# Kernel optimization log

Hardware: AMD Instinct MI355X
Metric: run time of the kernel (lower is better)

The kernel has to match this reference:

```python
import jax, jax.numpy as jnp
import numpy as np

N_NODES = 100000
N_EDGES = 1600000
D_IN = 64
D_OUT = 64
BN_EPS = 1e-5


def setup_inputs() -> dict:
    key = jax.random.key(0)
    k_x, k_src, k_dst, k_ew, k_w = jax.random.split(key, 5)
    x = jax.random.normal(k_x, (N_NODES, D_IN), dtype=jnp.float32)
    edge_src = jax.random.randint(k_src, (N_EDGES,), 0, N_NODES, dtype=jnp.int32)
    edge_dst = jax.random.randint(k_dst, (N_EDGES,), 0, N_NODES, dtype=jnp.int32)
    edge_weight = jax.random.uniform(k_ew, (N_EDGES,), dtype=jnp.float32)
    # Xavier-uniform weight, zero bias (reset_parameters)
    limit = float(np.sqrt(6.0 / (D_IN + D_OUT)))
    W = jax.random.uniform(k_w, (D_IN, D_OUT), dtype=jnp.float32, minval=-limit, maxval=limit)
    bias = jnp.zeros((D_OUT,), dtype=jnp.float32)
    gamma = jnp.ones((D_OUT,), dtype=jnp.float32)
    beta = jnp.zeros((D_OUT,), dtype=jnp.float32)
    return {"x": x, "edge_src": edge_src, "edge_dst": edge_dst,
            "edge_weight": edge_weight, "W": W, "bias": bias,
            "gamma": gamma, "beta": beta}


def reference(x, edge_src, edge_dst, edge_weight, W, bias, gamma, beta):
    # GraphConvolution: support = x @ W  -> [N, D_OUT]
    support = jnp.matmul(x, W)
    # spmm(adj, support) with adj in COO form: out[d] += w_e * support[s]
    msgs = edge_weight[:, None] * support[edge_src]        # [E, D_OUT]
    agg = jax.ops.segment_sum(msgs, edge_dst, num_segments=N_NODES)
    out = agg + bias
    # BatchNorm1d (training mode: batch statistics over node dim)
    mean = jnp.mean(out, axis=0)
    var = jnp.var(out, axis=0)
    out = (out - mean) * jax.lax.rsqrt(var + BN_EPS) * gamma + beta
    # ReLU activation; dropout is identity in deterministic/inference mode
    return jax.nn.relu(out)
```

## Files before the change

### kernel.cpp

```cpp
#include <hip/hip_runtime.h>
#include <hip/hip_bf16.h>

#define NN 100000
#define NE 1600000
#define DD 64
#define NCOARSE 98
#define GEMM_TILES 1563
#define PLACE_EPB 2048
#define PLACE_BLOCKS 782
#define LCNT_STRIDE 800
#define STAT_BLOCKS 256

__device__ inline unsigned short f2bf(float f) {
    __hip_bfloat16 h = __float2bfloat16(f);
    unsigned short s; __builtin_memcpy(&s, &h, 2); return s;
}
__device__ inline float pw(unsigned p) { return __uint_as_float((p & 0xFFFE0000u) >> 1); }

__global__ __launch_bounds__(256) void k_gemm(const float* __restrict__ x,
                                              const float* __restrict__ Wg,
                                              unsigned* __restrict__ support2) {
    __shared__ float Ws[DD * DD];
    __shared__ float Xs[64 * DD];
    const int r0 = blockIdx.x * 64;
    const int nrows = (r0 + 64 <= NN) ? 64 : (NN - r0);

    for (int i = threadIdx.x; i < DD * DD / 4; i += 256)
        ((float4*)Ws)[i] = ((const float4*)Wg)[i];
    const float4* xg = (const float4*)(x + (size_t)r0 * DD);
    for (int i = threadIdx.x; i < nrows * 16; i += 256)
        ((float4*)Xs)[i] = xg[i];
    __syncthreads();

    const int wave = threadIdx.x >> 6, lane = threadIdx.x & 63;
    const int half = lane >> 5, hl = lane & 31;
    const int rbase = wave * 16 + half * 8;

    float acc0[8] = {0.f, 0.f, 0.f, 0.f, 0.f, 0.f, 0.f, 0.f};
    float acc1[8] = {0.f, 0.f, 0.f, 0.f, 0.f, 0.f, 0.f, 0.f};
#pragma unroll 4
    for (int k = 0; k < DD; k += 4) {
        float2 w0 = *(const float2*)&Ws[(k + 0) * DD + 2 * hl];
        float2 w1 = *(const float2*)&Ws[(k + 1) * DD + 2 * hl];
        float2 w2 = *(const float2*)&Ws[(k + 2) * DD + 2 * hl];
        float2 w3 = *(const float2*)&Ws[(k + 3) * DD + 2 * hl];
#pragma unroll
        for (int r = 0; r < 8; ++r) {
            float4 xv = *(const float4*)&Xs[(rbase + r) * DD + k];
            acc0[r] = fmaf(xv.x, w0.x, acc0[r]); acc1[r] = fmaf(xv.x, w0.y, acc1[r]);
            acc0[r] = fmaf(xv.y, w1.x, acc0[r]); acc1[r] = fmaf(xv.y, w1.y, acc1[r]);
            acc0[r] = fmaf(xv.z, w2.x, acc0[r]); acc1[r] = fmaf(xv.z, w2.y, acc1[r]);
            acc0[r] = fmaf(xv.w, w3.x, acc0[r]); acc1[r] = fmaf(xv.w, w3.y, acc1[r]);
        }
    }
#pragma unroll
    for (int r = 0; r < 8; ++r) {
        const int row = rbase + r;
        if (row < nrows) {
            unsigned p = (unsigned)f2bf(acc0[r]) | ((unsigned)f2bf(acc1[r]) << 16);
            support2[(size_t)(r0 + row) * 32 + hl] = p;
        }
    }
}

__global__ __launch_bounds__(256) void k_pa_hist(const int* __restrict__ edst,
                                                 int* __restrict__ lcntT) {
    __shared__ int h[NCOARSE];
    for (int i = threadIdx.x; i < NCOARSE; i += 256) h[i] = 0;
    __syncthreads();
    const int e0 = blockIdx.x * PLACE_EPB;
#pragma unroll
    for (int k = 0; k < 8; ++k) {
        int e = e0 + k * 256 + threadIdx.x;
        if (e < NE) atomicAdd(&h[edst[e] >> 10], 1);
    }
    __syncthreads();
    for (int i = threadIdx.x; i < NCOARSE; i += 256)
        lcntT[i * LCNT_STRIDE + blockIdx.x] = h[i];
}

__global__ __launch_bounds__(256) void k_colscan(int* __restrict__ lcntT,
                                                 int* __restrict__ cnt98) {
    int* col = lcntT + blockIdx.x * LCNT_STRIDE;
    const int t = threadIdx.x, base = t * 4;
    int v[4], s = 0;
#pragma unroll
    for (int j = 0; j < 4; ++j) {
        v[j] = (base + j < PLACE_BLOCKS) ? col[base + j] : 0;
        s += v[j];
    }
    __shared__ int sc[256];
    sc[t] = s; __syncthreads();
    for (int o = 1; o < 256; o <<= 1) {
        int u = (t >= o) ? sc[t - o] : 0;
        __syncthreads();
        sc[t] += u;
        __syncthreads();
    }
    int run = sc[t] - s;
#pragma unroll
    for (int j = 0; j < 4; ++j) {
        if (base + j < PLACE_BLOCKS) col[base + j] = run;
        run += v[j];
    }
    if (t == 255) cnt98[blockIdx.x] = sc[255];
}

__global__ __launch_bounds__(128) void k_scan98(const int* __restrict__ cnt98,
                                                int* __restrict__ cstart,
                                                int* __restrict__ bstart) {
    __shared__ int sc[128];
    const int t = threadIdx.x;
    const int v = (t < NCOARSE) ? cnt98[t] : 0;
    sc[t] = v; __syncthreads();
    for (int o = 1; o < 128; o <<= 1) {
        int u = (t >= o) ? sc[t - o] : 0;
        __syncthreads();
        sc[t] += u;
        __syncthreads();
    }
    if (t < NCOARSE) cstart[t] = sc[t] - v;
    if (t == 0) { cstart[NCOARSE] = NE; bstart[NN] = NE; }
}

__global__ __launch_bounds__(256) void k_pa_scatter(const int* __restrict__ esrc,
                                                    const int* __restrict__ edst,
                                                    const float* __restrict__ ew,
                                                    const int* __restrict__ cstart,
                                                    const int* __restrict__ lcntT,
                                                    int2* __restrict__ permA) {
    __shared__ int loff[NCOARSE];
    for (int i = threadIdx.x; i < NCOARSE; i += 256)
        loff[i] = cstart[i] + lcntT[i * LCNT_STRIDE + blockIdx.x];
    __syncthreads();
    const int e0 = blockIdx.x * PLACE_EPB;
#pragma unroll
    for (int k = 0; k < 8; ++k) {
        int e = e0 + k * 256 + threadIdx.x;
        if (e < NE) {
            int d = edst[e];
            int p = atomicAdd(&loff[d >> 10], 1);
            permA[p] = make_int2(esrc[e] | ((d & 1023) << 20), __float_as_int(ew[e]));
        }
    }
}

__global__ __launch_bounds__(1024) void k_placeB(const int* __restrict__ cstart,
                                                 const int2* __restrict__ permA,
                                                 unsigned* __restrict__ perm,
                                                 int* __restrict__ bstart) {
    __shared__ int sc[1024], loff[1024];
    const int c = blockIdx.x, t = threadIdx.x;
    const int cs = cstart[c], ce = cstart[c + 1];
    sc[t] = 0;
    __syncthreads();
    for (int j = cs + t; j < ce; j += 1024)
        atomicAdd(&sc[(permA[j].x >> 20) & 1023], 1);
    __syncthreads();
    const int cnt = sc[t];
    for (int o = 1; o < 1024; o <<= 1) {
        int u = (t >= o) ? sc[t - o] : 0;
        __syncthreads();
        sc[t] += u;
        __syncthreads();
    }
    const int base = cs + sc[t] - cnt;
    loff[t] = base;
    const int node = c * 1024 + t;
    if (node < NN) bstart[node] = base;
    __syncthreads();
    for (int j = cs + t; j < ce; j += 1024) {
        int2 m = permA[j];
        int p = atomicAdd(&loff[(m.x >> 20) & 1023], 1);
        unsigned wb = (unsigned)(f2bf(__int_as_float(m.y)) & 0x7FFF);
        perm[p] = (unsigned)(m.x & 0x1FFFF) | (wb << 17);
    }
}

__global__ __launch_bounds__(256) void k_gather(const int* __restrict__ bstart,
                                                const unsigned* __restrict__ perm,
                                                const unsigned* __restrict__ support2,
                                                float* __restrict__ out) {
    const int wave = threadIdx.x >> 6, lane = threadIdx.x & 63;
    const int half = lane >> 5, hl = lane & 31;
    const int d = blockIdx.x * 4 + wave;
    const int bs = bstart[d], be = bstart[d + 1];
    float a0x = 0.f, a0y = 0.f, a1x = 0.f, a1y = 0.f;
    float a2x = 0.f, a2y = 0.f, a3x = 0.f, a3y = 0.f;
    int j0 = bs;
    for (; j0 + 7 < be; j0 += 8) {
        unsigned m0 = perm[j0 + half];
        unsigned m1 = perm[j0 + 2 + half];
        unsigned m2 = perm[j0 + 4 + half];
        unsigned m3 = perm[j0 + 6 + half];
        unsigned p0 = support2[(size_t)(m0 & 0x1FFFF) * 32 + hl];
        unsigned p1 = support2[(size_t)(m1 & 0x1FFFF) * 32 + hl];
        unsigned p2 = support2[(size_t)(m2 & 0x1FFFF) * 32 + hl];
        unsigned p3 = support2[(size_t)(m3 & 0x1FFFF) * 32 + hl];
        float w0 = pw(m0), w1 = pw(m1), w2 = pw(m2), w3 = pw(m3);
        a0x = fmaf(w0, __uint_as_float(p0 << 16), a0x);
        a0y = fmaf(w0, __uint_as_float(p0 & 0xffff0000u), a0y);
        a1x = fmaf(w1, __uint_as_float(p1 << 16), a1x);
        a1y = fmaf(w1, __uint_as_float(p1 & 0xffff0000u), a1y);
        a2x = fmaf(w2, __uint_as_float(p2 << 16), a2x);
        a2y = fmaf(w2, __uint_as_float(p2 & 0xffff0000u), a2y);
        a3x = fmaf(w3, __uint_as_float(p3 << 16), a3x);
        a3y = fmaf(w3, __uint_as_float(p3 & 0xffff0000u), a3y);
    }
    for (; j0 + 3 < be; j0 += 4) {
        unsigned m0 = perm[j0 + half];
        unsigned m1 = perm[j0 + 2 + half];
        unsigned p0 = support2[(size_t)(m0 & 0x1FFFF) * 32 + hl];
        unsigned p1 = support2[(size_t)(m1 & 0x1FFFF) * 32 + hl];
        float w0 = pw(m0), w1 = pw(m1);
        a0x = fmaf(w0, __uint_as_float(p0 << 16), a0x);
        a0y = fmaf(w0, __uint_as_float(p0 & 0xffff0000u), a0y);
        a1x = fmaf(w1, __uint_as_float(p1 << 16), a1x);
        a1y = fmaf(w1, __uint_as_float(p1 & 0xffff0000u), a1y);
    }
    for (; j0 + half < be; j0 += 2) {
        unsigned m = perm[j0 + half];
        unsigned p = support2[(size_t)(m & 0x1FFFF) * 32 + hl];
        float w = pw(m);
        a0x = fmaf(w, __uint_as_float(p << 16), a0x);
        a0y = fmaf(w, __uint_as_float(p & 0xffff0000u), a0y);
    }
    float ax = (a0x + a1x) + (a2x + a3x);
    float ay = (a0y + a1y) + (a2y + a3y);
    ax += __shfl_xor(ax, 32);
    ay += __shfl_xor(ay, 32);
    if (half == 0)
        *(float2*)(out + (size_t)d * DD + 2 * hl) = make_float2(ax, ay);
}

__device__ inline float4 shfl_down4(float4 v, int dd) {
    v.x = __shfl_down(v.x, dd, 64); v.y = __shfl_down(v.y, dd, 64);
    v.z = __shfl_down(v.z, dd, 64); v.w = __shfl_down(v.w, dd, 64);
    return v;
}
__device__ inline float4 add4(float4 a, float4 b) {
    a.x += b.x; a.y += b.y; a.z += b.z; a.w += b.w; return a;
}

__global__ __launch_bounds__(256) void k_stats(const float* __restrict__ agg,
                                               float* __restrict__ pstat) {
    const int lane = threadIdx.x & 63, wave = threadIdx.x >> 6;
    const int q = lane & 15, sub = lane >> 4;
    float4 s = {0, 0, 0, 0}, sq = {0, 0, 0, 0};
    const int stride = gridDim.x * 16;
    for (int row = (blockIdx.x * 4 + wave) * 4 + sub; row < NN; row += stride) {
        float4 v = *(const float4*)(agg + (size_t)row * DD + q * 4);
        s.x += v.x; s.y += v.y; s.z += v.z; s.w += v.w;
        sq.x = fmaf(v.x, v.x, sq.x); sq.y = fmaf(v.y, v.y, sq.y);
        sq.z = fmaf(v.z, v.z, sq.z); sq.w = fmaf(v.w, v.w, sq.w);
    }
    s = add4(s, shfl_down4(s, 32));  s = add4(s, shfl_down4(s, 16));
    sq = add4(sq, shfl_down4(sq, 32)); sq = add4(sq, shfl_down4(sq, 16));

    __shared__ float red[2][4][DD];
    if (lane < 16) {
        red[0][wave][q * 4 + 0] = s.x;  red[0][wave][q * 4 + 1] = s.y;
        red[0][wave][q * 4 + 2] = s.z;  red[0][wave][q * 4 + 3] = s.w;
        red[1][wave][q * 4 + 0] = sq.x; red[1][wave][q * 4 + 1] = sq.y;
        red[1][wave][q * 4 + 2] = sq.z; red[1][wave][q * 4 + 3] = sq.w;
    }
    __syncthreads();
    if (threadIdx.x < 2 * DD) {
        const int t = threadIdx.x;
        const int part = t >> 6, c = t & 63;
        pstat[blockIdx.x * 2 * DD + t] =
            red[part][0][c] + red[part][1][c] + red[part][2][c] + red[part][3][c];
    }
}

__global__ __launch_bounds__(128) void k_finstats(const float* __restrict__ pstat,
                                                  float* __restrict__ ss,
                                                  const float* __restrict__ gamma,
                                                  const float* __restrict__ beta) {
    const int t = threadIdx.x;
    float acc = 0.f;
    for (int b = 0; b < STAT_BLOCKS; ++b)
        acc += pstat[b * 2 * DD + t];
    __shared__ float red[2 * DD];
    red[t] = acc;
    __syncthreads();
    if (t < DD) {
        const float invn = 1.0f / NN;
        float mean = red[t] * invn;
        float var = fmaxf(red[DD + t] * invn - mean * mean, 0.f);
        float sc = rsqrtf(var + 1e-5f) * gamma[t];
        ss[t] = sc;
        ss[DD + t] = beta[t] - mean * sc;
    }
}

__global__ __launch_bounds__(256) void k_final(float* __restrict__ out,
                                               const float* __restrict__ ss) {
    const size_t idx = ((size_t)blockIdx.x * 256 + threadIdx.x) * 4;
    const int c = (int)(idx & 63);
    float4 v = *(const float4*)(out + idx);
    float4 o;
    o.x = fmaxf(fmaf(v.x, ss[c + 0], ss[DD + c + 0]), 0.f);
    o.y = fmaxf(fmaf(v.y, ss[c + 1], ss[DD + c + 1]), 0.f);
    o.z = fmaxf(fmaf(v.z, ss[c + 2], ss[DD + c + 2]), 0.f);
    o.w = fmaxf(fmaf(v.w, ss[c + 3], ss[DD + c + 3]), 0.f);
    *(float4*)(out + idx) = o;
}

extern "C" void kernel_launch(void* const* d_in, const int* in_sizes, int n_in,
                              void* d_out, int out_size, void* d_ws, size_t ws_size,
                              hipStream_t stream) {
    const float* x     = (const float*)d_in[0];
    const int*   esrc  = (const int*)d_in[1];
    const int*   edst  = (const int*)d_in[2];
    const float* ew    = (const float*)d_in[3];
    const float* W     = (const float*)d_in[4];
    const float* gamma = (const float*)d_in[6];
    const float* beta  = (const float*)d_in[7];
    float*       out   = (float*)d_out;

    char* ws = (char*)d_ws;
    unsigned* support2 = (unsigned*)ws;  ws += (size_t)NN * DD * 2;
    int2*     permA  = (int2*)ws;     ws += (size_t)NE * 8;
    unsigned* perm   = (unsigned*)ws; ws += (size_t)NE * 4;
    int*   lcntT  = (int*)ws;    ws += NCOARSE * LCNT_STRIDE * 4;
    int*   cnt98  = (int*)ws;    ws += NCOARSE * 4;
    float* ss     = (float*)ws;  ws += 128 * 4;
    int*   cstart = (int*)ws;    ws += (NCOARSE + 1) * 4;
    int*   bstart = (int*)ws;    ws += (NN + 4) * 4;
    float* pstat  = (float*)ws;  ws += STAT_BLOCKS * 2 * DD * 4;


    k_gemm      <<<GEMM_TILES, 256, 0, stream>>>(x, W, support2);
    k_pa_hist   <<<PLACE_BLOCKS, 256, 0, stream>>>(edst, lcntT);
    k_colscan   <<<NCOARSE, 256, 0, stream>>>(lcntT, cnt98);
    k_scan98    <<<1, 128, 0, stream>>>(cnt98, cstart, bstart);
    k_pa_scatter<<<PLACE_BLOCKS, 256, 0, stream>>>(esrc, edst, ew, cstart, lcntT, permA);
    k_placeB    <<<NCOARSE, 1024, 0, stream>>>(cstart, permA, perm, bstart);
    k_gather    <<<NN / 4, 256, 0, stream>>>(bstart, perm, support2, out);
    k_stats     <<<STAT_BLOCKS, 256, 0, stream>>>(out, pstat);
    k_finstats  <<<1, 128, 0, stream>>>(pstat, ss, gamma, beta);
    k_final     <<<NN * DD / 4 / 256, 256, 0, stream>>>(out, ss);
}
```

Baseline: 228.6 us.

## Merge GEMM and histogram launches, warp-shuffle scan in placeB, deeper gather unroll

Merges the GEMM and the coarse destination histogram into one launch, with extra blocks doing the histogram, so the independent work can overlap and one launch is saved. Replaces placeB's 1024-wide shared-memory Hillis-Steele scan, which needed many barriers, with a two-level wave-shuffle scan. Adds a 16-edge unrolled main loop to the gather so more loads are in flight per wave. The deeper unroll raises register pressure in the gather, and the merged kernel carries the histogram's shared array alongside the GEMM tiles.

```diff
diff --git a/kernel.cpp b/kernel.cpp
--- a/kernel.cpp
+++ b/kernel.cpp
@@ -17,9 +17,28 @@
 }
 __device__ inline float pw(unsigned p) { return __uint_as_float((p & 0xFFFE0000u) >> 1); }
 
-__global__ __launch_bounds__(256) void k_gemm(const float* __restrict__ x,
-                                              const float* __restrict__ Wg,
-                                              unsigned* __restrict__ support2) {
+__global__ __launch_bounds__(256) void k_gemm_hist(const float* __restrict__ x,
+                                                   const float* __restrict__ Wg,
+                                                   unsigned* __restrict__ support2,
+                                                   const int* __restrict__ edst,
+                                                   int* __restrict__ lcntT) {
+    if (blockIdx.x >= GEMM_TILES) {
+        __shared__ int h[NCOARSE];
+        const int blk = blockIdx.x - GEMM_TILES;
+        for (int i = threadIdx.x; i < NCOARSE; i += 256) h[i] = 0;
+        __syncthreads();
+        const int e0 = blk * PLACE_EPB;
+#pragma unroll
+        for (int k = 0; k < 8; ++k) {
+            int e = e0 + k * 256 + threadIdx.x;
+            if (e < NE) atomicAdd(&h[edst[e] >> 10], 1);
+        }
+        __syncthreads();
+        for (int i = threadIdx.x; i < NCOARSE; i += 256)
+            lcntT[i * LCNT_STRIDE + blk] = h[i];
+        return;
+    }
+
     __shared__ float Ws[DD * DD];
     __shared__ float Xs[64 * DD];
     const int r0 = blockIdx.x * 64;
@@ -61,22 +80,6 @@
             support2[(size_t)(r0 + row) * 32 + hl] = p;
         }
     }
-}
-
-__global__ __launch_bounds__(256) void k_pa_hist(const int* __restrict__ edst,
-                                                 int* __restrict__ lcntT) {
-    __shared__ int h[NCOARSE];
-    for (int i = threadIdx.x; i < NCOARSE; i += 256) h[i] = 0;
-    __syncthreads();
-    const int e0 = blockIdx.x * PLACE_EPB;
-#pragma unroll
-    for (int k = 0; k < 8; ++k) {
-        int e = e0 + k * 256 + threadIdx.x;
-        if (e < NE) atomicAdd(&h[edst[e] >> 10], 1);
-    }
-    __syncthreads();
-    for (int i = threadIdx.x; i < NCOARSE; i += 256)
-        lcntT[i * LCNT_STRIDE + blockIdx.x] = h[i];
 }
 
 __global__ __launch_bounds__(256) void k_colscan(int* __restrict__ lcntT,
@@ -149,22 +152,36 @@
                                                  const int2* __restrict__ permA,
                                                  unsigned* __restrict__ perm,
                                                  int* __restrict__ bstart) {
-    __shared__ int sc[1024], loff[1024];
+    __shared__ int sc[1024], loff[1024], wtot[16];
     const int c = blockIdx.x, t = threadIdx.x;
+    const int wave = t >> 6, lane = t & 63;
     const int cs = cstart[c], ce = cstart[c + 1];
     sc[t] = 0;
     __syncthreads();
     for (int j = cs + t; j < ce; j += 1024)
         atomicAdd(&sc[(permA[j].x >> 20) & 1023], 1);
     __syncthreads();
-    const int cnt = sc[t];
-    for (int o = 1; o < 1024; o <<= 1) {
-        int u = (t >= o) ? sc[t - o] : 0;
-        __syncthreads();
-        sc[t] += u;
-        __syncthreads();
-    }
-    const int base = cs + sc[t] - cnt;
+    const int v = sc[t];
+    int xv = v;
+#pragma unroll
+    for (int o = 1; o < 64; o <<= 1) {
+        int u = __shfl_up(xv, o, 64);
+        if (lane >= o) xv += u;
+    }
+    if (lane == 63) wtot[wave] = xv;
+    __syncthreads();
+    if (t < 16) {
+        int w = wtot[t];
+        int xw = w;
+#pragma unroll
+        for (int o = 1; o < 16; o <<= 1) {
+            int u = __shfl_up(xw, o, 64);
+            if (t >= o) xw += u;
+        }
+        wtot[t] = xw - w;
+    }
+    __syncthreads();
+    const int base = cs + wtot[wave] + xv - v;
     loff[t] = base;
     const int node = c * 1024 + t;
     if (node < NN) bstart[node] = base;
@@ -185,27 +202,34 @@
     const int half = lane >> 5, hl = lane & 31;
     const int d = blockIdx.x * 4 + wave;
     const int bs = bstart[d], be = bstart[d + 1];
-    float a0x = 0.f, a0y = 0.f, a1x = 0.f, a1y = 0.f;
-    float a2x = 0.f, a2y = 0.f, a3x = 0.f, a3y = 0.f;
+    float accx[4] = {0.f, 0.f, 0.f, 0.f};
+    float accy[4] = {0.f, 0.f, 0.f, 0.f};
     int j0 = bs;
+    for (; j0 + 15 < be; j0 += 16) {
+        unsigned m[8], p[8];
+#pragma unroll
+        for (int i = 0; i < 8; ++i) m[i] = perm[j0 + 2 * i + half];
+#pragma unroll
+        for (int i = 0; i < 8; ++i) p[i] = support2[(size_t)(m[i] & 0x1FFFF) * 32 + hl];
+#pragma unroll
+        for (int i = 0; i < 8; ++i) {
+            float w = pw(m[i]);
+            accx[i & 3] = fmaf(w, __uint_as_float(p[i] << 16), accx[i & 3]);
+            accy[i & 3] = fmaf(w, __uint_as_float(p[i] & 0xffff0000u), accy[i & 3]);
+        }
+    }
     for (; j0 + 7 < be; j0 += 8) {
-        unsigned m0 = perm[j0 + half];
-        unsigned m1 = perm[j0 + 2 + half];
-        unsigned m2 = perm[j0 + 4 + half];
-        unsigned m3 = perm[j0 + 6 + half];
-        unsigned p0 = support2[(size_t)(m0 & 0x1FFFF) * 32 + hl];
-        unsigned p1 = support2[(size_t)(m1 & 0x1FFFF) * 32 + hl];
-        unsigned p2 = support2[(size_t)(m2 & 0x1FFFF) * 32 + hl];
-        unsigned p3 = support2[(size_t)(m3 & 0x1FFFF) * 32 + hl];
-        float w0 = pw(m0), w1 = pw(m1), w2 = pw(m2), w3 = pw(m3);
-        a0x = fmaf(w0, __uint_as_float(p0 << 16), a0x);
-        a0y = fmaf(w0, __uint_as_float(p0 & 0xffff0000u), a0y);
-        a1x = fmaf(w1, __uint_as_float(p1 << 16), a1x);
-        a1y = fmaf(w1, __uint_as_float(p1 & 0xffff0000u), a1y);
-        a2x = fmaf(w2, __uint_as_float(p2 << 16), a2x);
-        a2y = fmaf(w2, __uint_as_float(p2 & 0xffff0000u), a2y);
-        a3x = fmaf(w3, __uint_as_float(p3 << 16), a3x);
-        a3y = fmaf(w3, __uint_as_float(p3 & 0xffff0000u), a3y);
+        unsigned m[4], p[4];
+#pragma unroll
+        for (int i = 0; i < 4; ++i) m[i] = perm[j0 + 2 * i + half];
+#pragma unroll
+        for (int i = 0; i < 4; ++i) p[i] = support2[(size_t)(m[i] & 0x1FFFF) * 32 + hl];
+#pragma unroll
+        for (int i = 0; i < 4; ++i) {
+            float w = pw(m[i]);
+            accx[i] = fmaf(w, __uint_as_float(p[i] << 16), accx[i]);
+            accy[i] = fmaf(w, __uint_as_float(p[i] & 0xffff0000u), accy[i]);
+        }
     }
     for (; j0 + 3 < be; j0 += 4) {
         unsigned m0 = perm[j0 + half];
@@ -213,20 +237,20 @@
         unsigned p0 = support2[(size_t)(m0 & 0x1FFFF) * 32 + hl];
         unsigned p1 = support2[(size_t)(m1 & 0x1FFFF) * 32 + hl];
         float w0 = pw(m0), w1 = pw(m1);
-        a0x = fmaf(w0, __uint_as_float(p0 << 16), a0x);
-        a0y = fmaf(w0, __uint_as_float(p0 & 0xffff0000u), a0y);
-        a1x = fmaf(w1, __uint_as_float(p1 << 16), a1x);
-        a1y = fmaf(w1, __uint_as_float(p1 & 0xffff0000u), a1y);
+        accx[0] = fmaf(w0, __uint_as_float(p0 << 16), accx[0]);
+        accy[0] = fmaf(w0, __uint_as_float(p0 & 0xffff0000u), accy[0]);
+        accx[1] = fmaf(w1, __uint_as_float(p1 << 16), accx[1]);
+        accy[1] = fmaf(w1, __uint_as_float(p1 & 0xffff0000u), accy[1]);
     }
     for (; j0 + half < be; j0 += 2) {
         unsigned m = perm[j0 + half];
         unsigned p = support2[(size_t)(m & 0x1FFFF) * 32 + hl];
         float w = pw(m);
-        a0x = fmaf(w, __uint_as_float(p << 16), a0x);
-        a0y = fmaf(w, __uint_as_float(p & 0xffff0000u), a0y);
-    }
-    float ax = (a0x + a1x) + (a2x + a3x);
-    float ay = (a0y + a1y) + (a2y + a3y);
+        accx[0] = fmaf(w, __uint_as_float(p << 16), accx[0]);
+        accy[0] = fmaf(w, __uint_as_float(p & 0xffff0000u), accy[0]);
+    }
+    float ax = (accx[0] + accx[1]) + (accx[2] + accx[3]);
+    float ay = (accy[0] + accy[1]) + (accy[2] + accy[3]);
     ax += __shfl_xor(ax, 32);
     ay += __shfl_xor(ay, 32);
     if (half == 0)
@@ -331,8 +355,7 @@
     float* pstat  = (float*)ws;  ws += STAT_BLOCKS * 2 * DD * 4;
 
 
-    k_gemm      <<<GEMM_TILES, 256, 0, stream>>>(x, W, support2);
-    k_pa_hist   <<<PLACE_BLOCKS, 256, 0, stream>>>(edst, lcntT);
+    k_gemm_hist <<<GEMM_TILES + PLACE_BLOCKS, 256, 0, stream>>>(x, W, support2, edst, lcntT);
     k_colscan   <<<NCOARSE, 256, 0, stream>>>(lcntT, cnt98);
     k_scan98    <<<1, 128, 0, stream>>>(cnt98, cstart, bstart);
     k_pa_scatter<<<PLACE_BLOCKS, 256, 0, stream>>>(esrc, edst, ew, cstart, lcntT, permA);
```

New measurement: 219.8 us. 1.04x faster.
